# Kernel optimization log

Measured on AMD Instinct MI355X. Metric: run time of the kernel, lower is better.

## Reference

```python
import jax, jax.numpy as jnp
import numpy as np

B, N, FIN, H, D = 4, 2048, 128, 4, 64
ALPHA = 0.2  # LeakyReLU negative slope


def _xavier_uniform(key, shape):
    fan_in, fan_out = shape[0], shape[1]
    limit = float(np.sqrt(6.0 / (fan_in + fan_out)))
    return jax.random.uniform(key, shape, jnp.float32, -limit, limit)


def setup_inputs() -> dict:
    key = jax.random.key(0)
    k1, k2, k3, k4 = jax.random.split(key, 4)
    x = jax.random.normal(k1, (B, N, FIN), jnp.float32)
    adj = jax.random.randint(k2, (B, N, N), 0, 2, jnp.int32)  # dense 0/1 mask
    W = _xavier_uniform(k3, (FIN, H * D))
    a = _xavier_uniform(k4, (2 * D, 1))
    return {"x": x, "adj": adj, "W": W, "a": a}


def reference(x, adj, W, a):
    Bb, Nn, _ = x.shape
    Dd = a.shape[0] // 2
    Hh = W.shape[1] // Dd
    # h: [B, N, H, D]
    h = (x @ W).reshape(Bb, Nn, Hh, Dd)
    # Additive attention: e[b,i,j,h] = leakyrelu(a1 . h[b,i,h] + a2 . h[b,j,h])
    a1 = a[:Dd, 0]
    a2 = a[Dd:, 0]
    ei = jnp.einsum('bnhd,d->bnh', h, a1)  # source (row i) term
    ej = jnp.einsum('bnhd,d->bnh', h, a2)  # dest (col j) term
    e = ei[:, :, None, :] + ej[:, None, :, :]  # [B, N, N, H]
    e = jnp.where(e >= 0, e, ALPHA * e)  # LeakyReLU
    e = jnp.where(adj[..., None] == 0, -jnp.inf, e)
    att = jax.nn.softmax(e, axis=2)  # softmax over neighbors j
    # dropout is a no-op in eval mode (training=False)
    out = jnp.einsum('bijh,bjhd->bihd', att, h)  # [B, N, H, D]
    return out.mean(axis=2)  # mean over heads -> [B, N, D]
```

## Files before the change

kernel.cpp:

```cpp
#include <hip/hip_runtime.h>

#define NN 2048
#define NH 4
#define DD 64
#define FIN 128
#define NB 4
#define LOG2E 1.44269504f

typedef unsigned short u16;
typedef unsigned int u32;
typedef short sh8 __attribute__((ext_vector_type(8)));
typedef float f32x4 __attribute__((ext_vector_type(4)));

static __device__ __forceinline__ u16 f2bf(float f) {
    u32 u = __builtin_bit_cast(u32, f);
    u += 0x7fffu + ((u >> 16) & 1u);
    return (u16)(u >> 16);
}
static __device__ __forceinline__ u32 pk_bf(float a, float b) {
    u32 ua = __builtin_bit_cast(u32, a) + 0x8000u;
    u32 ub = __builtin_bit_cast(u32, b) + 0x8000u;
    return __builtin_amdgcn_perm(ub, ua, 0x07060302u);
}
static __device__ __forceinline__ float fast_exp2(float x) {
    float r;
    asm("v_exp_f32 %0, %1" : "=v"(r) : "v"(x));
    return r;
}

static __device__ __forceinline__ void cd_probe(int ln15, int q, int* irow, int* icol) {
    sh8 pa, pb, qa, qb;
    #pragma unroll
    for (int ii = 0; ii < 8; ++ii) {
        pa[ii] = (short)f2bf((float)ln15);
        pb[ii] = 0;
        qa[ii] = 0;
        qb[ii] = (short)f2bf((float)ln15);
    }
    if (q == 0) { pb[0] = (short)f2bf(1.0f); qa[0] = (short)f2bf(1.0f); }
    f32x4 z = {};
    f32x4 prow = __builtin_amdgcn_mfma_f32_16x16x32_bf16(pa, pb, z, 0, 0, 0);
    f32x4 pcol = __builtin_amdgcn_mfma_f32_16x16x32_bf16(qa, qb, z, 0, 0, 0);
    #pragma unroll
    for (int r = 0; r < 4; ++r) {
        irow[r] = (int)(prow[r] + 0.5f);
        icol[r] = (int)(pcol[r] + 0.5f);
    }
}


__global__ __launch_bounds__(256)
void k_pack(const int* __restrict__ adj, const float* __restrict__ W,
            u32* __restrict__ msk, u16* __restrict__ WT) {
    const int tid = threadIdx.x;
    if (blockIdx.x < 2048) {
        const int wid  = (blockIdx.x * 256 + tid) >> 6;
        const int lane = tid & 63;
        for (int t = wid; t < NB * NN * 8; t += 8192) {
            const int c256 = t & 7;
            const int i    = (t >> 3) & (NN - 1);
            const int b    = t >> 14;
            const int4 v = *(const int4*)(adj + ((size_t)(b * NN + i)) * NN + c256 * 256 + lane * 4);
            u32 nib = (v.x ? 1u : 0u) | (v.y ? 2u : 0u) | (v.z ? 4u : 0u) | (v.w ? 8u : 0u);
            u32 w = nib << (4 * (lane & 7));
            w |= __shfl_xor(w, 1);
            w |= __shfl_xor(w, 2);
            w |= __shfl_xor(w, 4);
            if ((lane & 7) == 0)
                msk[((size_t)(b * 64 + c256 * 8 + (lane >> 3))) * NN + i] = w;
        }
    } else {
        const int bt  = blockIdx.x - 2048;
        const int kt  = bt & 3;
        const int ct8 = bt >> 2;
        __shared__ float tile[32][33];
        const int rr = tid >> 5, cc = tid & 31;
        #pragma unroll
        for (int i = 0; i < 4; ++i)
            tile[rr + 8 * i][cc] = W[(size_t)(kt * 32 + rr + 8 * i) * 256 + ct8 * 32 + cc];
        __syncthreads();
        #pragma unroll
        for (int i = 0; i < 4; ++i)
            WT[(size_t)(ct8 * 32 + rr + 8 * i) * FIN + kt * 32 + cc] = f2bf(tile[cc][rr + 8 * i]);
    }
}

__global__ __launch_bounds__(256)
void k_gemm_h(const float* __restrict__ x, const u16* __restrict__ WT,
              const float* __restrict__ a,
              u16* __restrict__ hTf, float* __restrict__ ei_g, float* __restrict__ ej_g) {
    const int nb = blockIdx.x, b = blockIdx.y;
    const int tid = threadIdx.x, hd = tid >> 6, lane = tid & 63, ln15 = lane & 15, q = lane >> 4;
    const int q8 = q * 8;
    const int n0 = nb * 64;

    __shared__ u16 xs[64][136];
    __shared__ float cs[NH][4][16][20];
    {
        const int col = (tid & 31) * 4;
        const int r0  = tid >> 5;
        #pragma unroll
        for (int rr = 0; rr < 8; ++rr) {
            const int row = r0 + rr * 8;
            const float4 v = *(const float4*)(x + ((size_t)(b * NN + n0 + row)) * FIN + col);
            *(u32*)&xs[row][col]     = pk_bf(v.x, v.y);
            *(u32*)&xs[row][col + 2] = pk_bf(v.z, v.w);
        }
    }
    __syncthreads();

    int irow[4], icol[4];
    cd_probe(ln15, q, irow, icol);

    f32x4 acc[4][4] = {};
    #pragma unroll
    for (int ks = 0; ks < 4; ++ks) {
        sh8 af[4], bfr[4];
        #pragma unroll
        for (int ct = 0; ct < 4; ++ct)
            af[ct] = *(const sh8*)(WT + (size_t)(hd * 64 + ct * 16 + ln15) * FIN + ks * 32 + q8);
        #pragma unroll
        for (int nt = 0; nt < 4; ++nt)
            bfr[nt] = *(const sh8*)&xs[nt * 16 + ln15][ks * 32 + q8];
        #pragma unroll
        for (int ct = 0; ct < 4; ++ct)
            #pragma unroll
            for (int nt = 0; nt < 4; ++nt)
                acc[ct][nt] = __builtin_amdgcn_mfma_f32_16x16x32_bf16(af[ct], bfr[nt], acc[ct][nt], 0, 0, 0);
    }

    float eip[4] = {}, ejq[4] = {};
    #pragma unroll
    for (int ct = 0; ct < 4; ++ct) {
        #pragma unroll
        for (int nt = 0; nt < 4; ++nt)
            #pragma unroll
            for (int r = 0; r < 4; ++r)
                cs[hd][nt][irow[r]][icol[r]] = acc[ct][nt][r];

        #pragma unroll
        for (int p = 0; p < 2; ++p) {
            const float4 c0 = *(const float4*)&cs[hd][2 * p + (q >> 1)][ln15][(q & 1) * 8];
            const float4 c1 = *(const float4*)&cs[hd][2 * p + (q >> 1)][ln15][(q & 1) * 8 + 4];
            uint4 o;
            o.x = pk_bf(c0.x, c0.y); o.y = pk_bf(c0.z, c0.w);
            o.z = pk_bf(c1.x, c1.y); o.w = pk_bf(c1.z, c1.w);
            *(uint4*)(hTf + ((((size_t)(b * NH + hd) * 64 + nb * 2 + p) * 4 + ct) * 512) + lane * 8) = o;
        }

        float a1v[4], a2v[4];
        #pragma unroll
        for (int r = 0; r < 4; ++r) {
            const int d = ct * 16 + 4 * q + r;
            a1v[r] = a[d] * LOG2E;
            a2v[r] = a[64 + d] * LOG2E;
        }
        #pragma unroll
        for (int nt = 0; nt < 4; ++nt)
            #pragma unroll
            for (int r = 0; r < 4; ++r) {
                const float v = cs[hd][nt][4 * q + r][ln15];
                eip[nt] += v * a1v[r];
                ejq[nt] += v * a2v[r];
            }
    }
    #pragma unroll
    for (int nt = 0; nt < 4; ++nt) {
        eip[nt] += __shfl_xor(eip[nt], 16);
        eip[nt] += __shfl_xor(eip[nt], 32);
        ejq[nt] += __shfl_xor(ejq[nt], 16);
        ejq[nt] += __shfl_xor(ejq[nt], 32);
    }
    if (lane < 16) {
        const size_t bhd = (size_t)(b * NH + hd) * NN;
        #pragma unroll
        for (int nt = 0; nt < 4; ++nt) {
            ei_g[bhd + n0 + nt * 16 + lane] = eip[nt];
            ej_g[bhd + n0 + nt * 16 + lane] = ejq[nt];
        }
    }
}

__global__ __launch_bounds__(256, 3)
void k_attn(const u32* __restrict__ msk, const u16* __restrict__ hTf,
            const float* __restrict__ ei_g, const float* __restrict__ ej_g,
            float* __restrict__ o_part, float* __restrict__ l_part, int nj) {
    const int ib = blockIdx.x, js = blockIdx.y, b = blockIdx.z;
    const int js_n = gridDim.y;
    const int tid = threadIdx.x, hd = tid >> 6, lane = tid & 63, ln15 = lane & 15, q = lane >> 4;
    const int q8 = q * 8;
    const int iA = ib * 32 + ln15;

    int irow[4], icol[4];
    cd_probe(ln15, q, irow, icol);

    const size_t bhd = (size_t)(b * NH + hd) * NN;
    const float eivA = ei_g[bhd + iA];
    const float eivB = ei_g[bhd + iA + 16];
    const u32*   mptr = msk + (size_t)(b * 64) * NN;
    const float* ejp  = ej_g + bhd + q8;
    const u16*   hfp  = hTf + (size_t)(b * NH + hd) * (64 * 2048) + (size_t)lane * 8;

    sh8 ones;
    #pragma unroll
    for (int ii = 0; ii < 8; ++ii) ones[ii] = (short)0x3F80;

    f32x4 acc[8] = {};
    f32x4 accl[2] = {};

    const int jt0 = js * nj;
    u32 mA = mptr[(size_t)jt0 * NN + iA];
    u32 mB = mptr[(size_t)jt0 * NN + iA + 16];
    float4 e0 = *(const float4*)(ejp + jt0 * 32);
    float4 e1 = *(const float4*)(ejp + jt0 * 32 + 4);
    sh8 h0 = *(const sh8*)(hfp + (size_t)jt0 * 2048);
    sh8 h1 = *(const sh8*)(hfp + (size_t)jt0 * 2048 + 512);
    sh8 h2 = *(const sh8*)(hfp + (size_t)jt0 * 2048 + 1024);
    sh8 h3 = *(const sh8*)(hfp + (size_t)jt0 * 2048 + 1536);

    for (int t = 0; t < nj; ++t) {
        const int tn = (t + 1 < nj) ? jt0 + t + 1 : jt0;
        const u32 mAn = mptr[(size_t)tn * NN + iA];
        const u32 mBn = mptr[(size_t)tn * NN + iA + 16];
        const float4 e0n = *(const float4*)(ejp + tn * 32);
        const float4 e1n = *(const float4*)(ejp + tn * 32 + 4);
        const sh8 h0n = *(const sh8*)(hfp + (size_t)tn * 2048);
        const sh8 h1n = *(const sh8*)(hfp + (size_t)tn * 2048 + 512);
        const sh8 h2n = *(const sh8*)(hfp + (size_t)tn * 2048 + 1024);
        const sh8 h3n = *(const sh8*)(hfp + (size_t)tn * 2048 + 1536);

        const float ef[8] = { e0.x, e0.y, e0.z, e0.w, e1.x, e1.y, e1.z, e1.w };
        const u32 mqA = mA >> q8;
        const u32 mqB = mB >> q8;
        float pA[8], pB[8];
        #pragma unroll
        for (int ii = 0; ii < 8; ++ii) {
            float eA = eivA + ef[ii];
            float eB = eivB + ef[ii];
            eA = fmaxf(eA, 0.2f * eA);
            eB = fmaxf(eB, 0.2f * eB);
            const float xA = fast_exp2(eA);
            const float xB = fast_exp2(eB);
            pA[ii] = (mqA & (1u << ii)) ? xA : 0.f;
            pB[ii] = (mqB & (1u << ii)) ? xB : 0.f;
        }
        union { uint4 u; sh8 v; } avA, avB;
        avA.u.x = pk_bf(pA[0], pA[1]); avA.u.y = pk_bf(pA[2], pA[3]);
        avA.u.z = pk_bf(pA[4], pA[5]); avA.u.w = pk_bf(pA[6], pA[7]);
        avB.u.x = pk_bf(pB[0], pB[1]); avB.u.y = pk_bf(pB[2], pB[3]);
        avB.u.z = pk_bf(pB[4], pB[5]); avB.u.w = pk_bf(pB[6], pB[7]);

        acc[0] = __builtin_amdgcn_mfma_f32_16x16x32_bf16(avA.v, h0, acc[0], 0, 0, 0);
        acc[1] = __builtin_amdgcn_mfma_f32_16x16x32_bf16(avA.v, h1, acc[1], 0, 0, 0);
        acc[2] = __builtin_amdgcn_mfma_f32_16x16x32_bf16(avA.v, h2, acc[2], 0, 0, 0);
        acc[3] = __builtin_amdgcn_mfma_f32_16x16x32_bf16(avA.v, h3, acc[3], 0, 0, 0);
        accl[0] = __builtin_amdgcn_mfma_f32_16x16x32_bf16(avA.v, ones, accl[0], 0, 0, 0);
        acc[4] = __builtin_amdgcn_mfma_f32_16x16x32_bf16(avB.v, h0, acc[4], 0, 0, 0);
        acc[5] = __builtin_amdgcn_mfma_f32_16x16x32_bf16(avB.v, h1, acc[5], 0, 0, 0);
        acc[6] = __builtin_amdgcn_mfma_f32_16x16x32_bf16(avB.v, h2, acc[6], 0, 0, 0);
        acc[7] = __builtin_amdgcn_mfma_f32_16x16x32_bf16(avB.v, h3, acc[7], 0, 0, 0);
        accl[1] = __builtin_amdgcn_mfma_f32_16x16x32_bf16(avB.v, ones, accl[1], 0, 0, 0);

        mA = mAn; mB = mBn; e0 = e0n; e1 = e1n;
        h0 = h0n; h1 = h1n; h2 = h2n; h3 = h3n;
    }

    const size_t pbA = (((size_t)b * 128 + ib * 2 + 0) * js_n + js) * NH + hd;
    const size_t pbB = (((size_t)b * 128 + ib * 2 + 1) * js_n + js) * NH + hd;
    #pragma unroll
    for (int r = 0; r < 4; ++r) {
        l_part[pbA * 16 + irow[r]] = accl[0][r];
        l_part[pbB * 16 + irow[r]] = accl[1][r];
    }
    float* opA = o_part + pbA * 1024;
    float* opB = o_part + pbB * 1024;
    #pragma unroll
    for (int dt = 0; dt < 4; ++dt)
        #pragma unroll
        for (int r = 0; r < 4; ++r) {
            opA[(size_t)irow[r] * 64 + dt * 16 + icol[r]] = acc[dt][r];
            opB[(size_t)irow[r] * 64 + dt * 16 + icol[r]] = acc[4 + dt][r];
        }
}

template <int JS>
__global__ __launch_bounds__(256)
void k_combine(const float* __restrict__ o_part, const float* __restrict__ l_part,
               float* __restrict__ out) {
    const int ib = blockIdx.x, b = blockIdx.y;
    const int tid = threadIdx.x;
    const int i = tid >> 4, d4 = (tid & 15) * 4;
    float  lv[NH][JS];
    float4 ov[NH][JS];
    #pragma unroll
    for (int h = 0; h < NH; ++h)
        #pragma unroll
        for (int js = 0; js < JS; ++js) {
            const size_t pbase = (((size_t)b * 128 + ib) * JS + js) * NH + h;
            lv[h][js] = l_part[pbase * 16 + i];
            ov[h][js] = *(const float4*)(o_part + pbase * 1024 + (size_t)i * 64 + d4);
        }
    float4 sacc = {0.f, 0.f, 0.f, 0.f};
    #pragma unroll
    for (int h = 0; h < NH; ++h) {
        float l = 0.f;
        float4 oh = {0.f, 0.f, 0.f, 0.f};
        #pragma unroll
        for (int js = 0; js < JS; ++js) {
            l += lv[h][js];
            oh.x += ov[h][js].x; oh.y += ov[h][js].y;
            oh.z += ov[h][js].z; oh.w += ov[h][js].w;
        }
        const float inv = 0.25f / l;
        sacc.x += oh.x * inv; sacc.y += oh.y * inv;
        sacc.z += oh.z * inv; sacc.w += oh.w * inv;
    }
    *(float4*)(out + ((size_t)(b * NN) + ib * 16 + i) * DD + d4) = sacc;
}

extern "C" void kernel_launch(void* const* d_in, const int* in_sizes, int n_in,
                              void* d_out, int out_size, void* d_ws, size_t ws_size,
                              hipStream_t stream) {
    const float* x = nullptr; const int* adj = nullptr;
    const float* W = nullptr; const float* a = nullptr;
    for (int i = 0; i < n_in; ++i) {
        switch (in_sizes[i]) {
            case NB * NN * FIN:  x   = (const float*)d_in[i]; break;
            case NB * NN * NN:   adj = (const int*)d_in[i];   break;
            case FIN * 256:      W   = (const float*)d_in[i]; break;
            case 2 * DD:         a   = (const float*)d_in[i]; break;
            default: break;
        }
    }
    if (!x)   x   = (const float*)d_in[0];
    if (!adj) adj = (const int*)d_in[1];
    if (!W)   W   = (const float*)d_in[2];
    if (!a)   a   = (const float*)d_in[3];
    float* out = (float*)d_out;

    char* ws = (char*)d_ws;
    u16*   WT  = (u16*)(ws);
    float* ei  = (float*)(ws + 65536);
    float* ej  = (float*)(ws + 196608);
    u16*   hTf = (u16*)(ws + 327680);
    u32*   msk = (u32*)(ws + 4521984);
    float* l_p = (float*)(ws + 6619136);
    float* o_p = (float*)(ws + 7143424);

    const size_t need4 = 7143424 + (size_t)4 * 8388608;
    const size_t need2 = 7143424 + (size_t)2 * 8388608;
    const int js_n = (ws_size >= need4) ? 4 : (ws_size >= need2) ? 2 : 1;

    k_pack<<<dim3(2080), dim3(256), 0, stream>>>(adj, W, msk, WT);
    k_gemm_h<<<dim3(32, NB), dim3(256), 0, stream>>>(x, WT, a, hTf, ei, ej);
    k_attn<<<dim3(64, js_n, NB), dim3(256), 0, stream>>>(msk, hTf, ei, ej, o_p, l_p, 64 / js_n);
    if (js_n == 4)      k_combine<4><<<dim3(128, NB), dim3(256), 0, stream>>>(o_p, l_p, out);
    else if (js_n == 2) k_combine<2><<<dim3(128, NB), dim3(256), 0, stream>>>(o_p, l_p, out);
    else                k_combine<1><<<dim3(128, NB), dim3(256), 0, stream>>>(o_p, l_p, out);
}
```

Measured before the change: 146.4 us.

## Fuse mask packing into attention and remove the j-split with its combine kernel

Removes the separate pack kernel: W is transposed and converted to bf16 inside each GEMM block's shared memory, and the adjacency bitmask is built per row-block in shared memory inside the attention kernel. The attention kernel no longer splits j across blocks, so the partial o/l buffers and the combine kernel go away and the head-mean normalisation happens in shared memory at the end. This cuts launches and global traffic for the intermediate mask and partials. In exchange only 256 attention blocks run with 1-block occupancy, which gives less parallelism to hide latency, and every GEMM block redundantly converts the whole of W.

```diff
diff --git a/kernel.cpp b/kernel.cpp
--- a/kernel.cpp
+++ b/kernel.cpp
@@ -50,57 +50,29 @@
 
 
 __global__ __launch_bounds__(256)
-void k_pack(const int* __restrict__ adj, const float* __restrict__ W,
-            u32* __restrict__ msk, u16* __restrict__ WT) {
-    const int tid = threadIdx.x;
-    if (blockIdx.x < 2048) {
-        const int wid  = (blockIdx.x * 256 + tid) >> 6;
-        const int lane = tid & 63;
-        for (int t = wid; t < NB * NN * 8; t += 8192) {
-            const int c256 = t & 7;
-            const int i    = (t >> 3) & (NN - 1);
-            const int b    = t >> 14;
-            const int4 v = *(const int4*)(adj + ((size_t)(b * NN + i)) * NN + c256 * 256 + lane * 4);
-            u32 nib = (v.x ? 1u : 0u) | (v.y ? 2u : 0u) | (v.z ? 4u : 0u) | (v.w ? 8u : 0u);
-            u32 w = nib << (4 * (lane & 7));
-            w |= __shfl_xor(w, 1);
-            w |= __shfl_xor(w, 2);
-            w |= __shfl_xor(w, 4);
-            if ((lane & 7) == 0)
-                msk[((size_t)(b * 64 + c256 * 8 + (lane >> 3))) * NN + i] = w;
-        }
-    } else {
-        const int bt  = blockIdx.x - 2048;
-        const int kt  = bt & 3;
-        const int ct8 = bt >> 2;
-        __shared__ float tile[32][33];
-        const int rr = tid >> 5, cc = tid & 31;
-        #pragma unroll
-        for (int i = 0; i < 4; ++i)
-            tile[rr + 8 * i][cc] = W[(size_t)(kt * 32 + rr + 8 * i) * 256 + ct8 * 32 + cc];
-        __syncthreads();
-        #pragma unroll
-        for (int i = 0; i < 4; ++i)
-            WT[(size_t)(ct8 * 32 + rr + 8 * i) * FIN + kt * 32 + cc] = f2bf(tile[cc][rr + 8 * i]);
-    }
-}
-
-__global__ __launch_bounds__(256)
-void k_gemm_h(const float* __restrict__ x, const u16* __restrict__ WT,
+void k_gemm_h(const float* __restrict__ x, const float* __restrict__ W,
               const float* __restrict__ a,
               u16* __restrict__ hTf, float* __restrict__ ei_g, float* __restrict__ ej_g) {
     const int nb = blockIdx.x, b = blockIdx.y;
     const int tid = threadIdx.x, hd = tid >> 6, lane = tid & 63, ln15 = lane & 15, q = lane >> 4;
     const int q8 = q * 8;
-    const int n0 = nb * 64;
-
-    __shared__ u16 xs[64][136];
-    __shared__ float cs[NH][4][16][20];
+    const int n0 = nb * 32;
+
+    __shared__ u16 WTs[256][136];
+    __shared__ u16 xs[32][136];
+    __shared__ float cs[NH][2][16][20];
+
+    {
+        const int c = tid;
+        #pragma unroll 8
+        for (int k = 0; k < FIN; ++k)
+            WTs[c][k] = f2bf(W[(size_t)k * 256 + c]);
+    }
     {
         const int col = (tid & 31) * 4;
         const int r0  = tid >> 5;
         #pragma unroll
-        for (int rr = 0; rr < 8; ++rr) {
+        for (int rr = 0; rr < 4; ++rr) {
             const int row = r0 + rr * 8;
             const float4 v = *(const float4*)(x + ((size_t)(b * NN + n0 + row)) * FIN + col);
             *(u32*)&xs[row][col]     = pk_bf(v.x, v.y);
@@ -112,40 +84,39 @@
     int irow[4], icol[4];
     cd_probe(ln15, q, irow, icol);
 
-    f32x4 acc[4][4] = {};
+    f32x4 acc[4][2] = {};
     #pragma unroll
     for (int ks = 0; ks < 4; ++ks) {
-        sh8 af[4], bfr[4];
+        sh8 af[4], bfr[2];
         #pragma unroll
         for (int ct = 0; ct < 4; ++ct)
-            af[ct] = *(const sh8*)(WT + (size_t)(hd * 64 + ct * 16 + ln15) * FIN + ks * 32 + q8);
-        #pragma unroll
-        for (int nt = 0; nt < 4; ++nt)
+            af[ct] = *(const sh8*)&WTs[hd * 64 + ct * 16 + ln15][ks * 32 + q8];
+        #pragma unroll
+        for (int nt = 0; nt < 2; ++nt)
             bfr[nt] = *(const sh8*)&xs[nt * 16 + ln15][ks * 32 + q8];
         #pragma unroll
         for (int ct = 0; ct < 4; ++ct)
             #pragma unroll
-            for (int nt = 0; nt < 4; ++nt)
+            for (int nt = 0; nt < 2; ++nt)
                 acc[ct][nt] = __builtin_amdgcn_mfma_f32_16x16x32_bf16(af[ct], bfr[nt], acc[ct][nt], 0, 0, 0);
     }
 
-    float eip[4] = {}, ejq[4] = {};
+    float eip[2] = {}, ejq[2] = {};
     #pragma unroll
     for (int ct = 0; ct < 4; ++ct) {
         #pragma unroll
-        for (int nt = 0; nt < 4; ++nt)
+        for (int nt = 0; nt < 2; ++nt)
             #pragma unroll
             for (int r = 0; r < 4; ++r)
                 cs[hd][nt][irow[r]][icol[r]] = acc[ct][nt][r];
 
-        #pragma unroll
-        for (int p = 0; p < 2; ++p) {
-            const float4 c0 = *(const float4*)&cs[hd][2 * p + (q >> 1)][ln15][(q & 1) * 8];
-            const float4 c1 = *(const float4*)&cs[hd][2 * p + (q >> 1)][ln15][(q & 1) * 8 + 4];
+        {
+            const float4 c0 = *(const float4*)&cs[hd][q >> 1][ln15][(q & 1) * 8];
+            const float4 c1 = *(const float4*)&cs[hd][q >> 1][ln15][(q & 1) * 8 + 4];
             uint4 o;
             o.x = pk_bf(c0.x, c0.y); o.y = pk_bf(c0.z, c0.w);
             o.z = pk_bf(c1.x, c1.y); o.w = pk_bf(c1.z, c1.w);
-            *(uint4*)(hTf + ((((size_t)(b * NH + hd) * 64 + nb * 2 + p) * 4 + ct) * 512) + lane * 8) = o;
+            *(uint4*)(hTf + ((((size_t)(b * NH + hd) * 64 + nb) * 4 + ct) * 512) + lane * 8) = o;
         }
 
         float a1v[4], a2v[4];
@@ -156,7 +127,7 @@
             a2v[r] = a[64 + d] * LOG2E;
         }
         #pragma unroll
-        for (int nt = 0; nt < 4; ++nt)
+        for (int nt = 0; nt < 2; ++nt)
             #pragma unroll
             for (int r = 0; r < 4; ++r) {
                 const float v = cs[hd][nt][4 * q + r][ln15];
@@ -165,7 +136,7 @@
             }
     }
     #pragma unroll
-    for (int nt = 0; nt < 4; ++nt) {
+    for (int nt = 0; nt < 2; ++nt) {
         eip[nt] += __shfl_xor(eip[nt], 16);
         eip[nt] += __shfl_xor(eip[nt], 32);
         ejq[nt] += __shfl_xor(ejq[nt], 16);
@@ -174,32 +145,50 @@
     if (lane < 16) {
         const size_t bhd = (size_t)(b * NH + hd) * NN;
         #pragma unroll
-        for (int nt = 0; nt < 4; ++nt) {
+        for (int nt = 0; nt < 2; ++nt) {
             ei_g[bhd + n0 + nt * 16 + lane] = eip[nt];
             ej_g[bhd + n0 + nt * 16 + lane] = ejq[nt];
         }
     }
 }
 
-__global__ __launch_bounds__(256, 3)
-void k_attn(const u32* __restrict__ msk, const u16* __restrict__ hTf,
+__global__ __launch_bounds__(256, 1)
+void k_attn(const int* __restrict__ adj, const u16* __restrict__ hTf,
             const float* __restrict__ ei_g, const float* __restrict__ ej_g,
-            float* __restrict__ o_part, float* __restrict__ l_part, int nj) {
-    const int ib = blockIdx.x, js = blockIdx.y, b = blockIdx.z;
-    const int js_n = gridDim.y;
+            float* __restrict__ out) {
+    const int ib = blockIdx.x, b = blockIdx.y;
     const int tid = threadIdx.x, hd = tid >> 6, lane = tid & 63, ln15 = lane & 15, q = lane >> 4;
     const int q8 = q * 8;
-    const int iA = ib * 32 + ln15;
+    const int i0 = ib * 32;
+
+    __shared__ u32 msk_s[64][32];
+    __shared__ float o_s[NH][32][68];
+    __shared__ float l_s[NH][32];
+
+    #pragma unroll
+    for (int rr = 0; rr < 8; ++rr) {
+        const int i = hd * 8 + rr;
+        #pragma unroll
+        for (int c256 = 0; c256 < 8; ++c256) {
+            const int4 v = *(const int4*)(adj + ((size_t)(b * NN + i0 + i)) * NN + c256 * 256 + lane * 4);
+            u32 nib = (v.x ? 1u : 0u) | (v.y ? 2u : 0u) | (v.z ? 4u : 0u) | (v.w ? 8u : 0u);
+            u32 w = nib << (4 * (lane & 7));
+            w |= __shfl_xor(w, 1);
+            w |= __shfl_xor(w, 2);
+            w |= __shfl_xor(w, 4);
+            if ((lane & 7) == 0) msk_s[c256 * 8 + (lane >> 3)][i] = w;
+        }
+    }
 
     int irow[4], icol[4];
     cd_probe(ln15, q, irow, icol);
+    __syncthreads();
 
     const size_t bhd = (size_t)(b * NH + hd) * NN;
-    const float eivA = ei_g[bhd + iA];
-    const float eivB = ei_g[bhd + iA + 16];
-    const u32*   mptr = msk + (size_t)(b * 64) * NN;
-    const float* ejp  = ej_g + bhd + q8;
-    const u16*   hfp  = hTf + (size_t)(b * NH + hd) * (64 * 2048) + (size_t)lane * 8;
+    const float eivA = ei_g[bhd + i0 + ln15];
+    const float eivB = ei_g[bhd + i0 + 16 + ln15];
+    const float* ejp = ej_g + bhd + q8;
+    const u16*   hfp = hTf + (size_t)(b * NH + hd) * (64 * 2048) + (size_t)lane * 8;
 
     sh8 ones;
     #pragma unroll
@@ -208,20 +197,15 @@
     f32x4 acc[8] = {};
     f32x4 accl[2] = {};
 
-    const int jt0 = js * nj;
-    u32 mA = mptr[(size_t)jt0 * NN + iA];
-    u32 mB = mptr[(size_t)jt0 * NN + iA + 16];
-    float4 e0 = *(const float4*)(ejp + jt0 * 32);
-    float4 e1 = *(const float4*)(ejp + jt0 * 32 + 4);
-    sh8 h0 = *(const sh8*)(hfp + (size_t)jt0 * 2048);
-    sh8 h1 = *(const sh8*)(hfp + (size_t)jt0 * 2048 + 512);
-    sh8 h2 = *(const sh8*)(hfp + (size_t)jt0 * 2048 + 1024);
-    sh8 h3 = *(const sh8*)(hfp + (size_t)jt0 * 2048 + 1536);
-
-    for (int t = 0; t < nj; ++t) {
-        const int tn = (t + 1 < nj) ? jt0 + t + 1 : jt0;
-        const u32 mAn = mptr[(size_t)tn * NN + iA];
-        const u32 mBn = mptr[(size_t)tn * NN + iA + 16];
+    float4 e0 = *(const float4*)(ejp);
+    float4 e1 = *(const float4*)(ejp + 4);
+    sh8 h0 = *(const sh8*)(hfp);
+    sh8 h1 = *(const sh8*)(hfp + 512);
+    sh8 h2 = *(const sh8*)(hfp + 1024);
+    sh8 h3 = *(const sh8*)(hfp + 1536);
+
+    for (int t = 0; t < 64; ++t) {
+        const int tn = (t + 1) & 63;
         const float4 e0n = *(const float4*)(ejp + tn * 32);
         const float4 e1n = *(const float4*)(ejp + tn * 32 + 4);
         const sh8 h0n = *(const sh8*)(hfp + (size_t)tn * 2048);
@@ -229,9 +213,9 @@
         const sh8 h2n = *(const sh8*)(hfp + (size_t)tn * 2048 + 1024);
         const sh8 h3n = *(const sh8*)(hfp + (size_t)tn * 2048 + 1536);
 
+        const u32 mqA = msk_s[t][ln15] >> q8;
+        const u32 mqB = msk_s[t][ln15 + 16] >> q8;
         const float ef[8] = { e0.x, e0.y, e0.z, e0.w, e1.x, e1.y, e1.z, e1.w };
-        const u32 mqA = mA >> q8;
-        const u32 mqB = mB >> q8;
         float pA[8], pB[8];
         #pragma unroll
         for (int ii = 0; ii < 8; ++ii) {
@@ -261,61 +245,44 @@
         acc[7] = __builtin_amdgcn_mfma_f32_16x16x32_bf16(avB.v, h3, acc[7], 0, 0, 0);
         accl[1] = __builtin_amdgcn_mfma_f32_16x16x32_bf16(avB.v, ones, accl[1], 0, 0, 0);
 
-        mA = mAn; mB = mBn; e0 = e0n; e1 = e1n;
+        e0 = e0n; e1 = e1n;
         h0 = h0n; h1 = h1n; h2 = h2n; h3 = h3n;
     }
 
-    const size_t pbA = (((size_t)b * 128 + ib * 2 + 0) * js_n + js) * NH + hd;
-    const size_t pbB = (((size_t)b * 128 + ib * 2 + 1) * js_n + js) * NH + hd;
     #pragma unroll
     for (int r = 0; r < 4; ++r) {
-        l_part[pbA * 16 + irow[r]] = accl[0][r];
-        l_part[pbB * 16 + irow[r]] = accl[1][r];
-    }
-    float* opA = o_part + pbA * 1024;
-    float* opB = o_part + pbB * 1024;
+        l_s[hd][irow[r]]      = accl[0][r];
+        l_s[hd][16 + irow[r]] = accl[1][r];
+    }
     #pragma unroll
     for (int dt = 0; dt < 4; ++dt)
         #pragma unroll
         for (int r = 0; r < 4; ++r) {
-            opA[(size_t)irow[r] * 64 + dt * 16 + icol[r]] = acc[dt][r];
-            opB[(size_t)irow[r] * 64 + dt * 16 + icol[r]] = acc[4 + dt][r];
-        }
-}
-
-template <int JS>
-__global__ __launch_bounds__(256)
-void k_combine(const float* __restrict__ o_part, const float* __restrict__ l_part,
-               float* __restrict__ out) {
-    const int ib = blockIdx.x, b = blockIdx.y;
-    const int tid = threadIdx.x;
-    const int i = tid >> 4, d4 = (tid & 15) * 4;
-    float  lv[NH][JS];
-    float4 ov[NH][JS];
-    #pragma unroll
-    for (int h = 0; h < NH; ++h)
-        #pragma unroll
-        for (int js = 0; js < JS; ++js) {
-            const size_t pbase = (((size_t)b * 128 + ib) * JS + js) * NH + h;
-            lv[h][js] = l_part[pbase * 16 + i];
-            ov[h][js] = *(const float4*)(o_part + pbase * 1024 + (size_t)i * 64 + d4);
-        }
-    float4 sacc = {0.f, 0.f, 0.f, 0.f};
-    #pragma unroll
-    for (int h = 0; h < NH; ++h) {
-        float l = 0.f;
-        float4 oh = {0.f, 0.f, 0.f, 0.f};
-        #pragma unroll
-        for (int js = 0; js < JS; ++js) {
-            l += lv[h][js];
-            oh.x += ov[h][js].x; oh.y += ov[h][js].y;
-            oh.z += ov[h][js].z; oh.w += ov[h][js].w;
-        }
-        const float inv = 0.25f / l;
-        sacc.x += oh.x * inv; sacc.y += oh.y * inv;
-        sacc.z += oh.z * inv; sacc.w += oh.w * inv;
-    }
-    *(float4*)(out + ((size_t)(b * NN) + ib * 16 + i) * DD + d4) = sacc;
+            o_s[hd][irow[r]][dt * 16 + icol[r]]      = acc[dt][r];
+            o_s[hd][16 + irow[r]][dt * 16 + icol[r]] = acc[4 + dt][r];
+        }
+    __syncthreads();
+
+    {
+        const int i  = tid >> 3;
+        const int d8 = (tid & 7) * 8;
+        float inv[NH];
+        #pragma unroll
+        for (int h = 0; h < NH; ++h) inv[h] = 0.25f / l_s[h][i];
+        float4 s0 = {0.f, 0.f, 0.f, 0.f}, s1 = {0.f, 0.f, 0.f, 0.f};
+        #pragma unroll
+        for (int h = 0; h < NH; ++h) {
+            const float4 v0 = *(const float4*)&o_s[h][i][d8];
+            const float4 v1 = *(const float4*)&o_s[h][i][d8 + 4];
+            s0.x += v0.x * inv[h]; s0.y += v0.y * inv[h];
+            s0.z += v0.z * inv[h]; s0.w += v0.w * inv[h];
+            s1.x += v1.x * inv[h]; s1.y += v1.y * inv[h];
+            s1.z += v1.z * inv[h]; s1.w += v1.w * inv[h];
+        }
+        float* op = out + ((size_t)(b * NN + i0 + i)) * DD + d8;
+        *(float4*)op = s0;
+        *(float4*)(op + 4) = s1;
+    }
 }
 
 extern "C" void kernel_launch(void* const* d_in, const int* in_sizes, int n_in,
@@ -339,22 +306,10 @@
     float* out = (float*)d_out;
 
     char* ws = (char*)d_ws;
-    u16*   WT  = (u16*)(ws);
-    float* ei  = (float*)(ws + 65536);
-    float* ej  = (float*)(ws + 196608);
-    u16*   hTf = (u16*)(ws + 327680);
-    u32*   msk = (u32*)(ws + 4521984);
-    float* l_p = (float*)(ws + 6619136);
-    float* o_p = (float*)(ws + 7143424);
-
-    const size_t need4 = 7143424 + (size_t)4 * 8388608;
-    const size_t need2 = 7143424 + (size_t)2 * 8388608;
-    const int js_n = (ws_size >= need4) ? 4 : (ws_size >= need2) ? 2 : 1;
-
-    k_pack<<<dim3(2080), dim3(256), 0, stream>>>(adj, W, msk, WT);
-    k_gemm_h<<<dim3(32, NB), dim3(256), 0, stream>>>(x, WT, a, hTf, ei, ej);
-    k_attn<<<dim3(64, js_n, NB), dim3(256), 0, stream>>>(msk, hTf, ei, ej, o_p, l_p, 64 / js_n);
-    if (js_n == 4)      k_combine<4><<<dim3(128, NB), dim3(256), 0, stream>>>(o_p, l_p, out);
-    else if (js_n == 2) k_combine<2><<<dim3(128, NB), dim3(256), 0, stream>>>(o_p, l_p, out);
-    else                k_combine<1><<<dim3(128, NB), dim3(256), 0, stream>>>(o_p, l_p, out);
-}
+    u16*   hTf = (u16*)(ws);
+    float* ei  = (float*)(ws + 4194304);
+    float* ej  = (float*)(ws + 4325376);
+
+    k_gemm_h<<<dim3(64, NB), dim3(256), 0, stream>>>(x, W, a, hTf, ei, ej);
+    k_attn<<<dim3(64, NB), dim3(256), 0, stream>>>(adj, hTf, ei, ej, out);
+}
```

Result: slower. 173.7 us (+18.6%).

## Fuse head combine into attention kernel and drop split-J partials

Applied to the files above, without the earlier changes.

The attention kernel now handles one 16-row tile over the full neighbour range instead of two row tiles over a split of the neighbour range. It reduces the four heads through shared memory and writes the normalised, head-averaged output directly. This removes the separate combine kernel and the global round trip of per-split partial outputs and row sums. In exchange, each block runs a longer serial loop, the grid is 512 blocks instead of up to 1024, each block does half the MFMA work per loaded h tile, and the occupancy hint is lowered.

```diff
diff --git a/kernel.cpp b/kernel.cpp
--- a/kernel.cpp
+++ b/kernel.cpp
@@ -181,23 +181,24 @@
     }
 }
 
-__global__ __launch_bounds__(256, 3)
+__global__ __launch_bounds__(256, 2)
 void k_attn(const u32* __restrict__ msk, const u16* __restrict__ hTf,
             const float* __restrict__ ei_g, const float* __restrict__ ej_g,
-            float* __restrict__ o_part, float* __restrict__ l_part, int nj) {
-    const int ib = blockIdx.x, js = blockIdx.y, b = blockIdx.z;
-    const int js_n = gridDim.y;
+            float* __restrict__ out) {
+    const int ib = blockIdx.x, b = blockIdx.y;
     const int tid = threadIdx.x, hd = tid >> 6, lane = tid & 63, ln15 = lane & 15, q = lane >> 4;
     const int q8 = q * 8;
-    const int iA = ib * 32 + ln15;
+    const int i0 = ib * 16;
+
+    __shared__ float o_s[NH][16][68];
+    __shared__ float l_s[NH][16];
 
     int irow[4], icol[4];
     cd_probe(ln15, q, irow, icol);
 
     const size_t bhd = (size_t)(b * NH + hd) * NN;
-    const float eivA = ei_g[bhd + iA];
-    const float eivB = ei_g[bhd + iA + 16];
-    const u32*   mptr = msk + (size_t)(b * 64) * NN;
+    const float eiv = ei_g[bhd + i0 + ln15];
+    const u32*   mptr = msk + (size_t)(b * 64) * NN + i0 + ln15;
     const float* ejp  = ej_g + bhd + q8;
     const u16*   hfp  = hTf + (size_t)(b * NH + hd) * (64 * 2048) + (size_t)lane * 8;
 
@@ -205,23 +206,20 @@
     #pragma unroll
     for (int ii = 0; ii < 8; ++ii) ones[ii] = (short)0x3F80;
 
-    f32x4 acc[8] = {};
-    f32x4 accl[2] = {};
-
-    const int jt0 = js * nj;
-    u32 mA = mptr[(size_t)jt0 * NN + iA];
-    u32 mB = mptr[(size_t)jt0 * NN + iA + 16];
-    float4 e0 = *(const float4*)(ejp + jt0 * 32);
-    float4 e1 = *(const float4*)(ejp + jt0 * 32 + 4);
-    sh8 h0 = *(const sh8*)(hfp + (size_t)jt0 * 2048);
-    sh8 h1 = *(const sh8*)(hfp + (size_t)jt0 * 2048 + 512);
-    sh8 h2 = *(const sh8*)(hfp + (size_t)jt0 * 2048 + 1024);
-    sh8 h3 = *(const sh8*)(hfp + (size_t)jt0 * 2048 + 1536);
-
-    for (int t = 0; t < nj; ++t) {
-        const int tn = (t + 1 < nj) ? jt0 + t + 1 : jt0;
-        const u32 mAn = mptr[(size_t)tn * NN + iA];
-        const u32 mBn = mptr[(size_t)tn * NN + iA + 16];
+    f32x4 acc[4] = {};
+    f32x4 accl = {};
+
+    u32 m = mptr[0];
+    float4 e0 = *(const float4*)(ejp);
+    float4 e1 = *(const float4*)(ejp + 4);
+    sh8 h0 = *(const sh8*)(hfp);
+    sh8 h1 = *(const sh8*)(hfp + 512);
+    sh8 h2 = *(const sh8*)(hfp + 1024);
+    sh8 h3 = *(const sh8*)(hfp + 1536);
+
+    for (int t = 0; t < 64; ++t) {
+        const int tn = (t + 1) & 63;
+        const u32 mn = mptr[(size_t)tn * NN];
         const float4 e0n = *(const float4*)(ejp + tn * 32);
         const float4 e1n = *(const float4*)(ejp + tn * 32 + 4);
         const sh8 h0n = *(const sh8*)(hfp + (size_t)tn * 2048);
@@ -230,92 +228,54 @@
         const sh8 h3n = *(const sh8*)(hfp + (size_t)tn * 2048 + 1536);
 
         const float ef[8] = { e0.x, e0.y, e0.z, e0.w, e1.x, e1.y, e1.z, e1.w };
-        const u32 mqA = mA >> q8;
-        const u32 mqB = mB >> q8;
-        float pA[8], pB[8];
+        const u32 mq = m >> q8;
+        float p[8];
         #pragma unroll
         for (int ii = 0; ii < 8; ++ii) {
-            float eA = eivA + ef[ii];
-            float eB = eivB + ef[ii];
-            eA = fmaxf(eA, 0.2f * eA);
-            eB = fmaxf(eB, 0.2f * eB);
-            const float xA = fast_exp2(eA);
-            const float xB = fast_exp2(eB);
-            pA[ii] = (mqA & (1u << ii)) ? xA : 0.f;
-            pB[ii] = (mqB & (1u << ii)) ? xB : 0.f;
-        }
-        union { uint4 u; sh8 v; } avA, avB;
-        avA.u.x = pk_bf(pA[0], pA[1]); avA.u.y = pk_bf(pA[2], pA[3]);
-        avA.u.z = pk_bf(pA[4], pA[5]); avA.u.w = pk_bf(pA[6], pA[7]);
-        avB.u.x = pk_bf(pB[0], pB[1]); avB.u.y = pk_bf(pB[2], pB[3]);
-        avB.u.z = pk_bf(pB[4], pB[5]); avB.u.w = pk_bf(pB[6], pB[7]);
-
-        acc[0] = __builtin_amdgcn_mfma_f32_16x16x32_bf16(avA.v, h0, acc[0], 0, 0, 0);
-        acc[1] = __builtin_amdgcn_mfma_f32_16x16x32_bf16(avA.v, h1, acc[1], 0, 0, 0);
-        acc[2] = __builtin_amdgcn_mfma_f32_16x16x32_bf16(avA.v, h2, acc[2], 0, 0, 0);
-        acc[3] = __builtin_amdgcn_mfma_f32_16x16x32_bf16(avA.v, h3, acc[3], 0, 0, 0);
-        accl[0] = __builtin_amdgcn_mfma_f32_16x16x32_bf16(avA.v, ones, accl[0], 0, 0, 0);
-        acc[4] = __builtin_amdgcn_mfma_f32_16x16x32_bf16(avB.v, h0, acc[4], 0, 0, 0);
-        acc[5] = __builtin_amdgcn_mfma_f32_16x16x32_bf16(avB.v, h1, acc[5], 0, 0, 0);
-        acc[6] = __builtin_amdgcn_mfma_f32_16x16x32_bf16(avB.v, h2, acc[6], 0, 0, 0);
-        acc[7] = __builtin_amdgcn_mfma_f32_16x16x32_bf16(avB.v, h3, acc[7], 0, 0, 0);
-        accl[1] = __builtin_amdgcn_mfma_f32_16x16x32_bf16(avB.v, ones, accl[1], 0, 0, 0);
-
-        mA = mAn; mB = mBn; e0 = e0n; e1 = e1n;
+            float e = eiv + ef[ii];
+            e = fmaxf(e, 0.2f * e);
+            const float ex = fast_exp2(e);
+            p[ii] = (mq & (1u << ii)) ? ex : 0.f;
+        }
+        union { uint4 u; sh8 v; } av;
+        av.u.x = pk_bf(p[0], p[1]); av.u.y = pk_bf(p[2], p[3]);
+        av.u.z = pk_bf(p[4], p[5]); av.u.w = pk_bf(p[6], p[7]);
+
+        acc[0] = __builtin_amdgcn_mfma_f32_16x16x32_bf16(av.v, h0, acc[0], 0, 0, 0);
+        acc[1] = __builtin_amdgcn_mfma_f32_16x16x32_bf16(av.v, h1, acc[1], 0, 0, 0);
+        acc[2] = __builtin_amdgcn_mfma_f32_16x16x32_bf16(av.v, h2, acc[2], 0, 0, 0);
+        acc[3] = __builtin_amdgcn_mfma_f32_16x16x32_bf16(av.v, h3, acc[3], 0, 0, 0);
+        accl   = __builtin_amdgcn_mfma_f32_16x16x32_bf16(av.v, ones, accl, 0, 0, 0);
+
+        m = mn; e0 = e0n; e1 = e1n;
         h0 = h0n; h1 = h1n; h2 = h2n; h3 = h3n;
     }
 
-    const size_t pbA = (((size_t)b * 128 + ib * 2 + 0) * js_n + js) * NH + hd;
-    const size_t pbB = (((size_t)b * 128 + ib * 2 + 1) * js_n + js) * NH + hd;
-    #pragma unroll
-    for (int r = 0; r < 4; ++r) {
-        l_part[pbA * 16 + irow[r]] = accl[0][r];
-        l_part[pbB * 16 + irow[r]] = accl[1][r];
-    }
-    float* opA = o_part + pbA * 1024;
-    float* opB = o_part + pbB * 1024;
+    #pragma unroll
+    for (int r = 0; r < 4; ++r)
+        l_s[hd][irow[r]] = accl[r];
     #pragma unroll
     for (int dt = 0; dt < 4; ++dt)
         #pragma unroll
-        for (int r = 0; r < 4; ++r) {
-            opA[(size_t)irow[r] * 64 + dt * 16 + icol[r]] = acc[dt][r];
-            opB[(size_t)irow[r] * 64 + dt * 16 + icol[r]] = acc[4 + dt][r];
-        }
-}
-
-template <int JS>
-__global__ __launch_bounds__(256)
-void k_combine(const float* __restrict__ o_part, const float* __restrict__ l_part,
-               float* __restrict__ out) {
-    const int ib = blockIdx.x, b = blockIdx.y;
-    const int tid = threadIdx.x;
-    const int i = tid >> 4, d4 = (tid & 15) * 4;
-    float  lv[NH][JS];
-    float4 ov[NH][JS];
-    #pragma unroll
-    for (int h = 0; h < NH; ++h)
-        #pragma unroll
-        for (int js = 0; js < JS; ++js) {
-            const size_t pbase = (((size_t)b * 128 + ib) * JS + js) * NH + h;
-            lv[h][js] = l_part[pbase * 16 + i];
-            ov[h][js] = *(const float4*)(o_part + pbase * 1024 + (size_t)i * 64 + d4);
-        }
-    float4 sacc = {0.f, 0.f, 0.f, 0.f};
-    #pragma unroll
-    for (int h = 0; h < NH; ++h) {
-        float l = 0.f;
-        float4 oh = {0.f, 0.f, 0.f, 0.f};
-        #pragma unroll
-        for (int js = 0; js < JS; ++js) {
-            l += lv[h][js];
-            oh.x += ov[h][js].x; oh.y += ov[h][js].y;
-            oh.z += ov[h][js].z; oh.w += ov[h][js].w;
-        }
-        const float inv = 0.25f / l;
-        sacc.x += oh.x * inv; sacc.y += oh.y * inv;
-        sacc.z += oh.z * inv; sacc.w += oh.w * inv;
-    }
-    *(float4*)(out + ((size_t)(b * NN) + ib * 16 + i) * DD + d4) = sacc;
+        for (int r = 0; r < 4; ++r)
+            o_s[hd][irow[r]][dt * 16 + icol[r]] = acc[dt][r];
+    __syncthreads();
+
+    {
+        const int i  = tid >> 4;
+        const int d4 = (tid & 15) * 4;
+        float inv[NH];
+        #pragma unroll
+        for (int h = 0; h < NH; ++h) inv[h] = 0.25f / l_s[h][i];
+        float4 s = {0.f, 0.f, 0.f, 0.f};
+        #pragma unroll
+        for (int h = 0; h < NH; ++h) {
+            const float4 v = *(const float4*)&o_s[h][i][d4];
+            s.x += v.x * inv[h]; s.y += v.y * inv[h];
+            s.z += v.z * inv[h]; s.w += v.w * inv[h];
+        }
+        *(float4*)(out + ((size_t)(b * NN + i0 + i)) * DD + d4) = s;
+    }
 }
 
 extern "C" void kernel_launch(void* const* d_in, const int* in_sizes, int n_in,
@@ -339,22 +299,13 @@
     float* out = (float*)d_out;
 
     char* ws = (char*)d_ws;
-    u16*   WT  = (u16*)(ws);
-    float* ei  = (float*)(ws + 65536);
-    float* ej  = (float*)(ws + 196608);
-    u16*   hTf = (u16*)(ws + 327680);
+    u16*   hTf = (u16*)(ws);
+    float* ei  = (float*)(ws + 4194304);
+    float* ej  = (float*)(ws + 4325376);
+    u16*   WT  = (u16*)(ws + 4456448);
     u32*   msk = (u32*)(ws + 4521984);
-    float* l_p = (float*)(ws + 6619136);
-    float* o_p = (float*)(ws + 7143424);
-
-    const size_t need4 = 7143424 + (size_t)4 * 8388608;
-    const size_t need2 = 7143424 + (size_t)2 * 8388608;
-    const int js_n = (ws_size >= need4) ? 4 : (ws_size >= need2) ? 2 : 1;
 
     k_pack<<<dim3(2080), dim3(256), 0, stream>>>(adj, W, msk, WT);
     k_gemm_h<<<dim3(32, NB), dim3(256), 0, stream>>>(x, WT, a, hTf, ei, ej);
-    k_attn<<<dim3(64, js_n, NB), dim3(256), 0, stream>>>(msk, hTf, ei, ej, o_p, l_p, 64 / js_n);
-    if (js_n == 4)      k_combine<4><<<dim3(128, NB), dim3(256), 0, stream>>>(o_p, l_p, out);
-    else if (js_n == 2) k_combine<2><<<dim3(128, NB), dim3(256), 0, stream>>>(o_p, l_p, out);
-    else                k_combine<1><<<dim3(128, NB), dim3(256), 0, stream>>>(o_p, l_p, out);
-}
+    k_attn<<<dim3(128, NB), dim3(256), 0, stream>>>(msk, hTf, ei, ej, out);
+}
```

Result: slower. 163.9 us (+11.9%).
